# Optimization experiments

Measured on AMD Instinct MI355X. Metric: run time of the kernel, lower is better.

## Reference

```python
import jax, jax.numpy as jnp
import numpy as np

B, S, H = 16, 512, 768
NH, HD = 12, 64  # num heads, head dim


def setup_inputs() -> dict:
    key = jax.random.key(0)
    ks = jax.random.split(key, 7)
    std = 0.02
    return {
        "hidden_state": jax.random.normal(ks[0], (B, S, H), dtype=jnp.float32),
        "attention_mask": jnp.ones((B, S), dtype=jnp.float32),
        "Wq": jax.random.normal(ks[1], (H, H), dtype=jnp.float32) * std,
        "bq": jnp.zeros((H,), dtype=jnp.float32),
        "Wk": jax.random.normal(ks[2], (H, H), dtype=jnp.float32) * std,
        "bk": jnp.zeros((H,), dtype=jnp.float32),
        "Wv": jax.random.normal(ks[3], (H, H), dtype=jnp.float32) * std,
        "bv": jnp.zeros((H,), dtype=jnp.float32),
    }


def reference(hidden_state, attention_mask, Wq, bq, Wk, bk, Wv, bv):
    b, s, h = hidden_state.shape
    scale = 1.0 / jnp.sqrt(jnp.asarray(HD, hidden_state.dtype))

    def split_heads(x):  # [B,S,H] -> [B,NH,S,HD]
        return x.reshape(b, s, NH, HD).transpose(0, 2, 1, 3)

    q = split_heads(hidden_state @ Wq.T + bq)
    k = split_heads(hidden_state @ Wk.T + bk)
    v = split_heads(hidden_state @ Wv.T + bv)

    # [B,NH,S,S]
    scores = jnp.einsum("bhqd,bhkd->bhqk", q, k) * scale
    mask_add = (1.0 - attention_mask)[:, None, None, :] * -10000.0
    probs = jax.nn.softmax(scores + mask_add, axis=-1)
    # dropout is identity in eval / deterministic reference

    ctx = jnp.einsum("bhqk,bhkd->bhqd", probs, v)
    ctx = ctx.transpose(0, 2, 1, 3).reshape(b, s, NH * HD)
    return ctx, probs
```

## Files before the change

### kernel.cpp

```cpp
#include <hip/hip_runtime.h>

namespace {
constexpr int kB  = 16;
constexpr int kS  = 512;
constexpr int kH  = 768;
constexpr int kNH = 12;
constexpr int kHD = 64;
constexpr int kM  = kB * kS;
}

typedef __attribute__((ext_vector_type(8))) short  short8;
typedef __attribute__((ext_vector_type(4))) float  f32x4;
typedef __attribute__((ext_vector_type(4))) unsigned short us4;
typedef __attribute__((ext_vector_type(2))) unsigned int   u32x2;

__device__ __forceinline__ unsigned short f2bf(float x) {
    unsigned u = __float_as_uint(x);
    return (unsigned short)((u + 0x7FFFu + ((u >> 16) & 1u)) >> 16);
}

__device__ __forceinline__ unsigned pack_bf16(float lo, float hi) {
    return (unsigned)f2bf(lo) | ((unsigned)f2bf(hi) << 16);
}

__device__ __forceinline__ void load_lds16(const unsigned short* g, unsigned short* l) {
    __builtin_amdgcn_global_load_lds(
        (const __attribute__((address_space(1))) void*)g,
        (__attribute__((address_space(3))) void*)l,
        16, 0, 0);
}

__global__ __launch_bounds__(256) void f32_to_bf16_kernel(
    const float* __restrict__ src, unsigned short* __restrict__ dst, int n4)
{
    int i = blockIdx.x * 256 + threadIdx.x;
    if (i >= n4) return;
    float4 v = reinterpret_cast<const float4*>(src)[i];
    us4 o;
    o.x = f2bf(v.x); o.y = f2bf(v.y); o.z = f2bf(v.z); o.w = f2bf(v.w);
    reinterpret_cast<us4*>(dst)[i] = o;
}

__global__ __launch_bounds__(256) void qkv_mfma_kernel(
    const unsigned short* __restrict__ hbf,
    const unsigned short* __restrict__ Wqb,
    const unsigned short* __restrict__ Wkb,
    const unsigned short* __restrict__ Wvb,
    const float* __restrict__ bq, const float* __restrict__ bk,
    const float* __restrict__ bv,
    unsigned short* __restrict__ qhi, unsigned short* __restrict__ qlo,
    unsigned short* __restrict__ khi, unsigned short* __restrict__ klo,
    unsigned short* __restrict__ vt)
{
    const int which = blockIdx.z;
    const unsigned short* W = (which == 0) ? Wqb : (which == 1) ? Wkb : Wvb;
    const float* bias       = (which == 0) ? bq  : (which == 1) ? bk  : bv;

    const int n0 = blockIdx.x * 128;
    const int m0 = blockIdx.y * 128;

    const int t    = threadIdx.x;
    const int lane = t & 63;
    const int w    = t >> 6;
    const int wm   = w >> 1;
    const int wn   = w & 1;

    __shared__ unsigned short As[128 * 32];
    __shared__ unsigned short Bs[128 * 32];

    f32x4 acc[4][4] = {};

    const int srow  = w * 32 + (lane >> 2);
    const int skoff = (lane & 3) * 8;
    const unsigned short* gA0 = hbf + (size_t)(m0 + srow) * kH + skoff;
    const unsigned short* gA1 = gA0 + (size_t)16 * kH;
    const unsigned short* gB0 = W   + (size_t)(n0 + srow) * kH + skoff;
    const unsigned short* gB1 = gB0 + (size_t)16 * kH;
    unsigned short* lA0 = &As[(w * 32) * 32];
    unsigned short* lA1 = &As[(w * 32 + 16) * 32];
    unsigned short* lB0 = &Bs[(w * 32) * 32];
    unsigned short* lB1 = &Bs[(w * 32 + 16) * 32];

    const int frow = lane & 15;
    const int fk   = (lane >> 4) * 8;

    for (int k0 = 0; k0 < kH; k0 += 32) {
        load_lds16(gA0 + k0, lA0);
        load_lds16(gA1 + k0, lA1);
        load_lds16(gB0 + k0, lB0);
        load_lds16(gB1 + k0, lB1);
        __syncthreads();

        short8 af[4], bf[4];
#pragma unroll
        for (int i = 0; i < 4; ++i)
            af[i] = *reinterpret_cast<const short8*>(
                &As[(wm * 64 + i * 16 + frow) * 32 + fk]);
#pragma unroll
        for (int j = 0; j < 4; ++j)
            bf[j] = *reinterpret_cast<const short8*>(
                &Bs[(wn * 64 + j * 16 + frow) * 32 + fk]);
#pragma unroll
        for (int i = 0; i < 4; ++i)
#pragma unroll
            for (int j = 0; j < 4; ++j)
                acc[i][j] = __builtin_amdgcn_mfma_f32_16x16x32_bf16(
                    af[i], bf[j], acc[i][j], 0, 0, 0);
        __syncthreads();
    }

    const int col = lane & 15;
    const int rq4 = (lane >> 4) << 2;

    if (which < 2) {
        unsigned short* ohi = which ? khi : qhi;
        unsigned short* olo = which ? klo : qlo;
#pragma unroll
        for (int j = 0; j < 4; ++j) {
            const int n  = n0 + wn * 64 + j * 16 + col;
            const float bj = bias[n];
            const int hh = n >> 6, d = n & 63;
#pragma unroll
            for (int i = 0; i < 4; ++i) {
                const int mrow = m0 + wm * 64 + i * 16 + rq4;
                const int bb = mrow >> 9;
                const int ss = mrow & 511;
                const size_t base =
                    ((size_t)(bb * kNH + hh) * kS + ss) * kHD + d;
#pragma unroll
                for (int r = 0; r < 4; ++r) {
                    float x = acc[i][j][r] + bj;
                    unsigned short hi = f2bf(x);
                    float res = x - __uint_as_float((unsigned)hi << 16);
                    ohi[base + (size_t)r * kHD] = hi;
                    olo[base + (size_t)r * kHD] = f2bf(res);
                }
            }
        }
    } else {
#pragma unroll
        for (int j = 0; j < 4; ++j) {
            const int n  = n0 + wn * 64 + j * 16 + col;
            const float bj = bias[n];
            const int hh = n >> 6, d = n & 63;
#pragma unroll
            for (int i = 0; i < 4; ++i) {
                const int mrow = m0 + wm * 64 + i * 16 + rq4;
                const int bb = mrow >> 9;
                const int ss = mrow & 511;
                us4 o;
                o.x = f2bf(acc[i][j][0] + bj);
                o.y = f2bf(acc[i][j][1] + bj);
                o.z = f2bf(acc[i][j][2] + bj);
                o.w = f2bf(acc[i][j][3] + bj);
                *reinterpret_cast<us4*>(
                    &vt[((size_t)(bb * kNH + hh) * kHD + d) * kS + ss]) = o;
            }
        }
    }
}

__global__ __launch_bounds__(256) void attn_kernel(
    const unsigned short* __restrict__ qhi, const unsigned short* __restrict__ qlo,
    const unsigned short* __restrict__ khi, const unsigned short* __restrict__ klo,
    const unsigned short* __restrict__ vtp, const float* __restrict__ mask,
    float* __restrict__ ctx, float* __restrict__ probs)
{
    const int bid = blockIdx.x;
    const int swz = (bid & 7) * 192 + (bid >> 3);
    const int qt  = swz & 7;
    const int bh  = swz >> 3;
    const int b   = bh / kNH;
    const int h   = bh % kNH;
    const int q0  = qt * 64;

    const int t    = threadIdx.x;
    const int lane = t & 63;
    const int w    = t >> 6;
    const int g    = lane >> 4;
    const int fr   = lane & 15;

    __shared__ unsigned short Khs[2][4096];
    __shared__ unsigned short Kls[2][4096];
    __shared__ unsigned short Vts[2][4096];
    __shared__ unsigned int   Pp[4][576];

    const int qrow = q0 + w * 16 + fr;
    const unsigned short* qh = qhi + ((size_t)bh * kS + qrow) * kHD + g * 8;
    const unsigned short* ql = qlo + ((size_t)bh * kS + qrow) * kHD + g * 8;
    const short8 qfh0 = *reinterpret_cast<const short8*>(qh);
    const short8 qfh1 = *reinterpret_cast<const short8*>(qh + 32);
    const short8 qfl0 = *reinterpret_cast<const short8*>(ql);
    const short8 qfl1 = *reinterpret_cast<const short8*>(ql + 32);

    const int c0 = (w * 2 + 0) * 64 + lane;
    const int c1 = (w * 2 + 1) * 64 + lane;
    const int r0 = c0 >> 3, r1 = c1 >> 3;
    const int s0b = ((c0 & 7) * 16) ^ ((r0 & 7) << 4);
    const int s1b = ((c1 & 7) * 16) ^ ((r1 & 7) << 4);
    const int ko0 = r0 * 128 + s0b,  ko1 = r1 * 128 + s1b;
    const int vo0 = r0 * 1024 + s0b, vo1 = r1 * 1024 + s1b;
    const char* kh_b = (const char*)(khi + (size_t)bh * kS * kHD);
    const char* kl_b = (const char*)(klo + (size_t)bh * kS * kHD);
    const char* vt_b = (const char*)(vtp + (size_t)bh * kHD * kS);
    const int l0 = (w * 2 + 0) * 512;
    const int l1 = (w * 2 + 1) * 512;

    unsigned pk[8][4][2];
    f32x4 cacc[4] = {};
    float rs = 0.0f;
    const float* mrow = mask + b * kS;

    load_lds16((const unsigned short*)(kh_b + ko0), &Khs[0][l0]);
    load_lds16((const unsigned short*)(kh_b + ko1), &Khs[0][l1]);
    load_lds16((const unsigned short*)(kl_b + ko0), &Kls[0][l0]);
    load_lds16((const unsigned short*)(kl_b + ko1), &Kls[0][l1]);
    load_lds16((const unsigned short*)(vt_b + vo0), &Vts[0][l0]);
    load_lds16((const unsigned short*)(vt_b + vo1), &Vts[0][l1]);

#pragma unroll
    for (int kt = 0; kt < 8; ++kt) {
        const int cur = kt & 1;
        __syncthreads();

        if (kt < 7) {
            const int nxt = cur ^ 1;
            load_lds16((const unsigned short*)(kh_b + (kt + 1) * 8192 + ko0), &Khs[nxt][l0]);
            load_lds16((const unsigned short*)(kh_b + (kt + 1) * 8192 + ko1), &Khs[nxt][l1]);
            load_lds16((const unsigned short*)(kl_b + (kt + 1) * 8192 + ko0), &Kls[nxt][l0]);
            load_lds16((const unsigned short*)(kl_b + (kt + 1) * 8192 + ko1), &Kls[nxt][l1]);
            load_lds16((const unsigned short*)(vt_b + (kt + 1) * 128 + vo0), &Vts[nxt][l0]);
            load_lds16((const unsigned short*)(vt_b + (kt + 1) * 128 + vo1), &Vts[nxt][l1]);
        }

        __builtin_amdgcn_s_setprio(1);

#pragma unroll
        for (int ks = 0; ks < 4; ++ks) {
            f32x4 sa = {};
#pragma unroll
            for (int d2 = 0; d2 < 2; ++d2) {
                const int kr  = ks * 16 + fr;
                const int off = kr * 128 + ((d2 * 64 + g * 16) ^ ((kr & 7) << 4));
                short8 ah = *reinterpret_cast<const short8*>((const char*)Khs[cur] + off);
                short8 al = *reinterpret_cast<const short8*>((const char*)Kls[cur] + off);
                const short8 qhf = d2 ? qfh1 : qfh0;
                const short8 qlf = d2 ? qfl1 : qfl0;
                sa = __builtin_amdgcn_mfma_f32_16x16x32_bf16(ah, qhf, sa, 0, 0, 0);
                sa = __builtin_amdgcn_mfma_f32_16x16x32_bf16(ah, qlf, sa, 0, 0, 0);
                sa = __builtin_amdgcn_mfma_f32_16x16x32_bf16(al, qhf, sa, 0, 0, 0);
            }
            const float4 mv = *reinterpret_cast<const float4*>(
                &mrow[kt * 64 + ks * 16 + g * 4]);
            float p0 = __expf(fmaf(sa[0], 0.125f, fmaf(mv.x, 1e4f, -1e4f)));
            float p1 = __expf(fmaf(sa[1], 0.125f, fmaf(mv.y, 1e4f, -1e4f)));
            float p2 = __expf(fmaf(sa[2], 0.125f, fmaf(mv.z, 1e4f, -1e4f)));
            float p3 = __expf(fmaf(sa[3], 0.125f, fmaf(mv.w, 1e4f, -1e4f)));
            rs += (p0 + p1) + (p2 + p3);
            const unsigned u0 = pack_bf16(p0, p1);
            const unsigned u1 = pack_bf16(p2, p3);
            pk[kt][ks][0] = u0;
            pk[kt][ks][1] = u1;
            *reinterpret_cast<u32x2*>(&Pp[w][fr * 36 + ks * 8 + g * 2]) =
                (u32x2){u0, u1};
        }

#pragma unroll
        for (int kp = 0; kp < 2; ++kp) {
            short8 pa = *reinterpret_cast<const short8*>(
                &Pp[w][fr * 36 + kp * 16 + g * 4]);
#pragma unroll
            for (int dt = 0; dt < 4; ++dt) {
                const int vr  = dt * 16 + fr;
                const int off = vr * 128 + ((kp * 64 + g * 16) ^ ((vr & 7) << 4));
                short8 vb = *reinterpret_cast<const short8*>((const char*)Vts[cur] + off);
                cacc[dt] = __builtin_amdgcn_mfma_f32_16x16x32_bf16(
                    pa, vb, cacc[dt], 0, 0, 0);
            }
        }

        __builtin_amdgcn_s_setprio(0);
    }

    rs += __shfl_xor(rs, 16, 64);
    rs += __shfl_xor(rs, 32, 64);
    const float inv = 1.0f / rs;

    float* prow = probs + ((size_t)bh * kS + qrow) * kS;
#pragma unroll
    for (int kt = 0; kt < 8; ++kt)
#pragma unroll
        for (int ks = 0; ks < 4; ++ks) {
            const unsigned u0 = pk[kt][ks][0], u1 = pk[kt][ks][1];
            f32x4 o;
            o.x = __uint_as_float(u0 << 16) * inv;
            o.y = __uint_as_float(u0 & 0xFFFF0000u) * inv;
            o.z = __uint_as_float(u1 << 16) * inv;
            o.w = __uint_as_float(u1 & 0xFFFF0000u) * inv;
            __builtin_nontemporal_store(
                o, reinterpret_cast<f32x4*>(prow + kt * 64 + ks * 16 + g * 4));
        }

    float invr[4];
#pragma unroll
    for (int r = 0; r < 4; ++r) invr[r] = __shfl(inv, g * 4 + r, 64);
    float* crow = ctx + ((size_t)(b * kS + q0 + w * 16 + g * 4)) * kH
                      + h * kHD + fr;
#pragma unroll
    for (int dt = 0; dt < 4; ++dt)
#pragma unroll
        for (int r = 0; r < 4; ++r)
            __builtin_nontemporal_store(cacc[dt][r] * invr[r],
                                        crow + (size_t)r * kH + dt * 16);
}

extern "C" void kernel_launch(void* const* d_in, const int* in_sizes, int n_in,
                              void* d_out, int out_size, void* d_ws, size_t ws_size,
                              hipStream_t stream) {
    (void)in_sizes; (void)n_in; (void)out_size; (void)ws_size;

    const float* hidden = (const float*)d_in[0];
    const float* mask   = (const float*)d_in[1];
    const float* Wq     = (const float*)d_in[2];
    const float* bq     = (const float*)d_in[3];
    const float* Wk     = (const float*)d_in[4];
    const float* bk     = (const float*)d_in[5];
    const float* Wv     = (const float*)d_in[6];
    const float* bv     = (const float*)d_in[7];

    float* ctx   = (float*)d_out;
    float* probs = (float*)d_out + (size_t)kB * kS * kH;

    unsigned short* hbf = (unsigned short*)d_ws;
    unsigned short* wqb = hbf + (size_t)kM * kH;
    unsigned short* wkb = wqb + (size_t)kH * kH;
    unsigned short* wvb = wkb + (size_t)kH * kH;
    unsigned short* qhi = wvb + (size_t)kH * kH;
    const size_t nqkv = (size_t)kB * kNH * kS * kHD;
    unsigned short* qlo = qhi + nqkv;
    unsigned short* khi = qlo + nqkv;
    unsigned short* klo = khi + nqkv;
    unsigned short* vt  = klo + nqkv;

    const int nh4 = (kM * kH) / 4;
    const int nw4 = (kH * kH) / 4;
    f32_to_bf16_kernel<<<nh4 / 256, 256, 0, stream>>>(hidden, hbf, nh4);
    f32_to_bf16_kernel<<<nw4 / 256, 256, 0, stream>>>(Wq, wqb, nw4);
    f32_to_bf16_kernel<<<nw4 / 256, 256, 0, stream>>>(Wk, wkb, nw4);
    f32_to_bf16_kernel<<<nw4 / 256, 256, 0, stream>>>(Wv, wvb, nw4);

    dim3 gp(kH / 128, kM / 128, 3);
    qkv_mfma_kernel<<<gp, 256, 0, stream>>>(hbf, wqb, wkb, wvb,
                                            bq, bk, bv,
                                            qhi, qlo, khi, klo, vt);

    attn_kernel<<<dim3(kB * kNH * (kS / 64)), 256, 0, stream>>>(
        qhi, qlo, khi, klo, vt, mask, ctx, probs);
}
```

Before: 399.0 us.

## Merge bf16 conversion launches and widen QKV GEMM K-tile with XOR-swizzled LDS

The four f32-to-bf16 conversion launches are folded into a single kernel that dispatches on the global index, which removes launch overhead. The QKV GEMM now stages a 64-wide K slice per iteration instead of 32. That halves the number of barriers and loop iterations and gives two MFMA k-steps per sync. LDS rows are XOR-swizzled in 16-byte units to avoid bank conflicts on fragment reads, at the cost of double the LDS footprint per block.

```diff
diff --git a/kernel.cpp b/kernel.cpp
--- a/kernel.cpp
+++ b/kernel.cpp
@@ -30,15 +30,31 @@
         16, 0, 0);
 }
 
-__global__ __launch_bounds__(256) void f32_to_bf16_kernel(
-    const float* __restrict__ src, unsigned short* __restrict__ dst, int n4)
+__global__ __launch_bounds__(256) void cvt_all_kernel(
+    const float* __restrict__ hidden, const float* __restrict__ Wq,
+    const float* __restrict__ Wk, const float* __restrict__ Wv,
+    unsigned short* __restrict__ hbf, unsigned short* __restrict__ wqb,
+    unsigned short* __restrict__ wkb, unsigned short* __restrict__ wvb)
 {
+    const int nH4 = (kM * kH) / 4;
+    const int nW4 = (kH * kH) / 4;
     int i = blockIdx.x * 256 + threadIdx.x;
-    if (i >= n4) return;
-    float4 v = reinterpret_cast<const float4*>(src)[i];
+    const float* src;
+    unsigned short* dst;
+    int off;
+    if (i < nH4) {
+        src = hidden; dst = hbf; off = i;
+    } else {
+        int j = i - nH4;
+        int which = j / nW4;
+        off = j - which * nW4;
+        src = (which == 0) ? Wq : (which == 1) ? Wk : Wv;
+        dst = (which == 0) ? wqb : (which == 1) ? wkb : wvb;
+    }
+    float4 v = reinterpret_cast<const float4*>(src)[off];
     us4 o;
     o.x = f2bf(v.x); o.y = f2bf(v.y); o.z = f2bf(v.z); o.w = f2bf(v.w);
-    reinterpret_cast<us4*>(dst)[i] = o;
+    reinterpret_cast<us4*>(dst)[off] = o;
 }
 
 __global__ __launch_bounds__(256) void qkv_mfma_kernel(
@@ -65,47 +81,48 @@
     const int wm   = w >> 1;
     const int wn   = w & 1;
 
-    __shared__ unsigned short As[128 * 32];
-    __shared__ unsigned short Bs[128 * 32];
+    __shared__ unsigned short As[128 * 64];
+    __shared__ unsigned short Bs[128 * 64];
 
     f32x4 acc[4][4] = {};
 
-    const int srow  = w * 32 + (lane >> 2);
-    const int skoff = (lane & 3) * 8;
-    const unsigned short* gA0 = hbf + (size_t)(m0 + srow) * kH + skoff;
-    const unsigned short* gA1 = gA0 + (size_t)16 * kH;
-    const unsigned short* gB0 = W   + (size_t)(n0 + srow) * kH + skoff;
-    const unsigned short* gB1 = gB0 + (size_t)16 * kH;
-    unsigned short* lA0 = &As[(w * 32) * 32];
-    unsigned short* lA1 = &As[(w * 32 + 16) * 32];
-    unsigned short* lB0 = &Bs[(w * 32) * 32];
-    unsigned short* lB1 = &Bs[(w * 32 + 16) * 32];
+    const int row8  = lane >> 3;
+    const int sunit = (lane & 7) ^ row8;
+    const unsigned short* gA = hbf + (size_t)(m0 + w * 32 + row8) * kH + sunit * 8;
+    const unsigned short* gB = W   + (size_t)(n0 + w * 32 + row8) * kH + sunit * 8;
 
     const int frow = lane & 15;
     const int fk   = (lane >> 4) * 8;
-
-    for (int k0 = 0; k0 < kH; k0 += 32) {
-        load_lds16(gA0 + k0, lA0);
-        load_lds16(gA1 + k0, lA1);
-        load_lds16(gB0 + k0, lB0);
-        load_lds16(gB1 + k0, lB1);
+    const int fswz = (frow & 7) << 3;
+
+    for (int k0 = 0; k0 < kH; k0 += 64) {
+#pragma unroll
+        for (int i = 0; i < 4; ++i) {
+            load_lds16(gA + k0 + (size_t)(8 * i) * kH, &As[(w * 32 + 8 * i) * 64]);
+            load_lds16(gB + k0 + (size_t)(8 * i) * kH, &Bs[(w * 32 + 8 * i) * 64]);
+        }
         __syncthreads();
 
-        short8 af[4], bf[4];
-#pragma unroll
-        for (int i = 0; i < 4; ++i)
-            af[i] = *reinterpret_cast<const short8*>(
-                &As[(wm * 64 + i * 16 + frow) * 32 + fk]);
-#pragma unroll
-        for (int j = 0; j < 4; ++j)
-            bf[j] = *reinterpret_cast<const short8*>(
-                &Bs[(wn * 64 + j * 16 + frow) * 32 + fk]);
-#pragma unroll
-        for (int i = 0; i < 4; ++i)
+        short8 af[2][4], bf[2][4];
+#pragma unroll
+        for (int kk = 0; kk < 2; ++kk) {
+#pragma unroll
+            for (int i = 0; i < 4; ++i)
+                af[kk][i] = *reinterpret_cast<const short8*>(
+                    &As[(wm * 64 + i * 16 + frow) * 64 + ((kk * 32 + fk) ^ fswz)]);
 #pragma unroll
             for (int j = 0; j < 4; ++j)
-                acc[i][j] = __builtin_amdgcn_mfma_f32_16x16x32_bf16(
-                    af[i], bf[j], acc[i][j], 0, 0, 0);
+                bf[kk][j] = *reinterpret_cast<const short8*>(
+                    &Bs[(wn * 64 + j * 16 + frow) * 64 + ((kk * 32 + fk) ^ fswz)]);
+        }
+#pragma unroll
+        for (int kk = 0; kk < 2; ++kk)
+#pragma unroll
+            for (int i = 0; i < 4; ++i)
+#pragma unroll
+                for (int j = 0; j < 4; ++j)
+                    acc[i][j] = __builtin_amdgcn_mfma_f32_16x16x32_bf16(
+                        af[kk][i], bf[kk][j], acc[i][j], 0, 0, 0);
         __syncthreads();
     }
 
@@ -342,12 +359,9 @@
     unsigned short* klo = khi + nqkv;
     unsigned short* vt  = klo + nqkv;
 
-    const int nh4 = (kM * kH) / 4;
-    const int nw4 = (kH * kH) / 4;
-    f32_to_bf16_kernel<<<nh4 / 256, 256, 0, stream>>>(hidden, hbf, nh4);
-    f32_to_bf16_kernel<<<nw4 / 256, 256, 0, stream>>>(Wq, wqb, nw4);
-    f32_to_bf16_kernel<<<nw4 / 256, 256, 0, stream>>>(Wk, wkb, nw4);
-    f32_to_bf16_kernel<<<nw4 / 256, 256, 0, stream>>>(Wv, wvb, nw4);
+    const int ncvt = ((kM * kH) / 4 + 3 * (kH * kH) / 4) / 256;
+    cvt_all_kernel<<<ncvt, 256, 0, stream>>>(hidden, Wq, Wk, Wv,
+                                             hbf, wqb, wkb, wvb);
 
     dim3 gp(kH / 128, kM / 128, 3);
     qkv_mfma_kernel<<<gp, 256, 0, stream>>>(hbf, wqb, wkb, wvb,
```

Result: faster. 383.7 us (-3.8%).
